# Optimization experiments

Measured on AMD Instinct MI355X. Metric: run time of the kernel, lower is better.

Reference implementation:

```python
import jax, jax.numpy as jnp
import numpy as np

NUM_HEADS = 8
NUM_LANDMARKS = 64
TOPK_LANDMARKS = 4


def setup_inputs() -> dict:
    key = jax.random.key(0)
    k1, k2, k3, k4 = jax.random.split(key, 4)
    B, N, C = 1, 2048, 512
    return {
        "x": jax.random.normal(k1, (B, N, C), jnp.float32),
        "w_qkv": jax.random.normal(k2, (3 * C, C), jnp.float32) * 0.02,
        "w_proj": jax.random.normal(k3, (C, C), jnp.float32) * 0.02,
        "b_proj": jax.random.normal(k4, (C,), jnp.float32) * 0.02,
    }


def reference(x, w_qkv, w_proj, b_proj):
    B, N, C = x.shape
    H = NUM_HEADS
    Dh = C // H
    m = min(NUM_LANDMARKS, N)          # number of segments (torch views (B,H,m,seg,D))
    kl = min(TOPK_LANDMARKS, m)
    scale = Dh ** -0.5

    qkv = (x @ w_qkv.T).reshape(B, N, 3, H, Dh).transpose(2, 0, 3, 1, 4)
    q, k, v = qkv[0], qkv[1], qkv[2]   # each (B,H,N,Dh)

    seg = -(-N // m)                   # segment length = ceil(N/m)
    pad = seg * m - N

    def segmentize(t):
        if pad > 0:
            t = jnp.pad(t, ((0, 0), (0, 0), (0, pad), (0, 0)))
        return t.reshape(B, H, m, seg, Dh)

    k_seg = segmentize(k)              # (B,H,m,seg,Dh)
    v_seg = segmentize(v)

    centroids = k_seg.mean(axis=3)     # (B,H,m,Dh) -- includes pad zeros, as in torch
    route = jnp.einsum('bhnd,bhmd->bhnm', q, centroids) * scale
    _, topk_idx = jax.lax.top_k(route, kl)  # (B,H,N,kl)

    # gather routed segments per query: (B,H,N,kl,seg,Dh)
    gather = jax.vmap(jax.vmap(lambda segs, ix: segs[ix]))
    sel_k = gather(k_seg, topk_idx).reshape(B, H, N, kl * seg, Dh)
    sel_v = gather(v_seg, topk_idx).reshape(B, H, N, kl * seg, Dh)

    attn = jnp.einsum('bhnd,bhnkd->bhnk', q, sel_k) * scale
    attn = jax.nn.softmax(attn, axis=-1)
    out = jnp.einsum('bhnk,bhnkd->bhnd', attn, sel_v)  # (B,H,N,Dh)
    out = out.transpose(0, 2, 1, 3).reshape(B, N, C)
    return out @ w_proj.T + b_proj
```

## Files before the change

kernel.cpp:

```cpp
#include <hip/hip_runtime.h>
#include <hip/hip_bf16.h>
#include <math.h>

#define N_TOK 2048
#define C_DIM 512
#define H_NUM 8
#define DH 64
#define M_LM 64
#define SEG 32
#define KL 4
#define SCALE 0.125f

typedef __attribute__((ext_vector_type(8))) short short8;
typedef __attribute__((ext_vector_type(8))) unsigned short ushort8v;
typedef __attribute__((ext_vector_type(4))) float f32x4;

__device__ inline unsigned short f2bf(float f) {
  unsigned u = __float_as_uint(f);
  u += 0x7FFF + ((u >> 16) & 1);
  return (unsigned short)(u >> 16);
}
__device__ inline float bf2f(unsigned short h) {
  return __uint_as_float(((unsigned)h) << 16);
}

__global__ __launch_bounds__(256) void gemm_qk(
    const float* __restrict__ A, const float* __restrict__ B,
    float* __restrict__ out_q, float* __restrict__ out_k)
{
  __shared__ float As[32][68];
  __shared__ float Bs[32][68];
  int tid = threadIdx.x;
  int tx = tid & 15, ty = tid >> 4;
  int row0 = blockIdx.y << 6;
  int col0 = blockIdx.x << 6;
  float acc[4][4] = {};
  int kk = tid & 31, rr = tid >> 5;

  float pa[8], pb[8];
#pragma unroll
  for (int i = 0; i < 8; i++) {
    pa[i] = A[(size_t)(row0 + rr + i * 8) * 512 + kk];
    pb[i] = B[(size_t)(col0 + rr + i * 8) * 512 + kk];
  }

  for (int k0 = 0; k0 < 512; k0 += 32) {
    __syncthreads();
#pragma unroll
    for (int i = 0; i < 8; i++) {
      As[kk][rr + i * 8] = pa[i];
      Bs[kk][rr + i * 8] = pb[i];
    }
    __syncthreads();
    if (k0 + 32 < 512) {
#pragma unroll
      for (int i = 0; i < 8; i++) {
        pa[i] = A[(size_t)(row0 + rr + i * 8) * 512 + k0 + 32 + kk];
        pb[i] = B[(size_t)(col0 + rr + i * 8) * 512 + k0 + 32 + kk];
      }
    }
#pragma unroll
    for (int kk2 = 0; kk2 < 32; kk2++) {
      float a[4], b[4];
      *(float4*)a = *(const float4*)&As[kk2][ty << 2];
      *(float4*)b = *(const float4*)&Bs[kk2][tx << 2];
#pragma unroll
      for (int i = 0; i < 4; i++)
#pragma unroll
        for (int j = 0; j < 4; j++) acc[i][j] += a[i] * b[j];
    }
  }

  int t = col0 >> 9;
  int h = (col0 >> 6) & 7;
  float* dst = (t == 0) ? out_q : out_k;
#pragma unroll
  for (int i = 0; i < 4; i++) {
    int n = row0 + (ty << 2) + i;
#pragma unroll
    for (int j = 0; j < 4; j++) {
      int d = (tx << 2) + j;
      dst[(size_t)((h << 11) + n) * DH + d] = acc[i][j];
    }
  }
}

__global__ void split3_kernel(const float* __restrict__ x, const float* __restrict__ wv,
                              const float* __restrict__ wp,
                              unsigned short* __restrict__ X2,
                              unsigned short* __restrict__ W2v,
                              unsigned short* __restrict__ WP2)
{
  int idx = blockIdx.x * 256 + threadIdx.x;
  const float* src; unsigned short* dst; int li;
  if (idx < 1048576)      { src = x;  dst = X2;  li = idx; }
  else if (idx < 1310720) { src = wv; dst = W2v; li = idx - 1048576; }
  else                    { src = wp; dst = WP2; li = idx - 1310720; }
  int r = li >> 9, k = li & 511;
  float a = src[li];
  unsigned short h1 = f2bf(a);
  float r1 = a - bf2f(h1);
  dst[(size_t)(r << 10) + k] = h1;
  dst[(size_t)(r << 10) + 512 + k] = f2bf(r1);
}

__global__ __launch_bounds__(256) void gemm_mfma(
    const unsigned short* __restrict__ A2, const unsigned short* __restrict__ B2,
    unsigned short* __restrict__ ov16, float* __restrict__ ofull,
    const float* __restrict__ bias, int ldout, int mode)
{
  __shared__ short Al[4096];
  __shared__ short Bl[4096];
  int tid = threadIdx.x;
  int lane = tid & 63, w = tid >> 6;
  int row0 = blockIdx.y << 6, col0 = blockIdx.x << 6;
  int wr = (w >> 1) * 32, wc = (w & 1) * 32;
  int m_lo = tid & 7, h8 = (tid >> 3) & 7, m_hi = tid >> 6;
  int ms = m_hi * 8 + m_lo;
  int q = lane >> 4, ln = lane & 15;

  f32x4 acc[2][2];
#pragma unroll
  for (int mi = 0; mi < 2; mi++)
#pragma unroll
    for (int ni = 0; ni < 2; ni++)
#pragma unroll
      for (int r = 0; r < 4; r++) acc[mi][ni][r] = 0.0f;

  for (int s = 0; s < 24; s++) {
    int ka = (s < 8) ? s * 64 : (s < 16) ? 512 + (s - 8) * 64 : (s - 16) * 64;
    int kb = (s < 8) ? s * 64 : (s < 16) ? (s - 8) * 64 : 512 + (s - 16) * 64;
    short8 a0 = *(const short8*)(A2 + (size_t)(row0 + ms) * 1024 + ka + h8 * 8);
    short8 a1 = *(const short8*)(A2 + (size_t)(row0 + ms + 32) * 1024 + ka + h8 * 8);
    short8 b0 = *(const short8*)(B2 + (size_t)(col0 + ms) * 1024 + kb + h8 * 8);
    short8 b1 = *(const short8*)(B2 + (size_t)(col0 + ms + 32) * 1024 + kb + h8 * 8);
    __syncthreads();
    *(short8*)&Al[(h8 * 64 + ms) * 8] = a0;
    *(short8*)&Al[(h8 * 64 + ms + 32) * 8] = a1;
    *(short8*)&Bl[(h8 * 64 + ms) * 8] = b0;
    *(short8*)&Bl[(h8 * 64 + ms + 32) * 8] = b1;
    __syncthreads();
    short8 af[2][2], bf[2][2];
#pragma unroll
    for (int sub = 0; sub < 2; sub++)
#pragma unroll
      for (int i = 0; i < 2; i++) {
        af[sub][i] = *(const short8*)&Al[((sub * 4 + q) * 64 + wr + i * 16 + ln) * 8];
        bf[sub][i] = *(const short8*)&Bl[((sub * 4 + q) * 64 + wc + i * 16 + ln) * 8];
      }
#pragma unroll
    for (int sub = 0; sub < 2; sub++)
#pragma unroll
      for (int mi = 0; mi < 2; mi++)
#pragma unroll
        for (int ni = 0; ni < 2; ni++)
          acc[mi][ni] = __builtin_amdgcn_mfma_f32_16x16x32_bf16(
              af[sub][mi], bf[sub][ni], acc[mi][ni], 0, 0, 0);
  }

  if (mode == 0) {
    int hh = (col0 >> 6) & 7;
#pragma unroll
    for (int mi = 0; mi < 2; mi++)
#pragma unroll
      for (int ni = 0; ni < 2; ni++)
#pragma unroll
        for (int r = 0; r < 4; r++) {
          int row = row0 + wr + mi * 16 + q * 4 + r;
          int d = wc + ni * 16 + ln;
          ov16[(size_t)((hh << 11) + row) * DH + d] = f2bf(acc[mi][ni][r]);
        }
  } else {
#pragma unroll
    for (int mi = 0; mi < 2; mi++)
#pragma unroll
      for (int ni = 0; ni < 2; ni++)
#pragma unroll
        for (int r = 0; r < 4; r++) {
          int row = row0 + wr + mi * 16 + q * 4 + r;
          int col = col0 + wc + ni * 16 + ln;
          ofull[(size_t)row * ldout + col] = acc[mi][ni][r] + bias[col];
        }
  }
}

__global__ void centroid_kernel(const float* __restrict__ kb, float* __restrict__ cent)
{
  int idx = blockIdx.x * blockDim.x + threadIdx.x;
  int m = (idx >> 6) & 63;
  int h = idx >> 12;
  int d = idx & 63;
  const float* base = kb + ((size_t)(h << 11) + m * SEG) * DH + d;
  float s = 0.f;
#pragma unroll
  for (int ss = 0; ss < SEG; ss++) s += base[(size_t)ss * DH];
  cent[idx] = s * (1.0f / SEG);
}

__global__ void kbf_kernel(const float* __restrict__ kb, unsigned short* __restrict__ kbf)
{
  int idx = blockIdx.x * 256 + threadIdx.x;
  float4 v = ((const float4*)kb)[idx];
  ushort4 o;
  o.x = f2bf(v.x); o.y = f2bf(v.y); o.z = f2bf(v.z); o.w = f2bf(v.w);
  ((ushort4*)kbf)[idx] = o;
}

__global__ __launch_bounds__(256) void route_topk_kernel(
    const float* __restrict__ qb, const float* __restrict__ cent, int* __restrict__ topk)
{
  __shared__ float centT[64][65];
  __shared__ float qs[4][64];
  int tid = threadIdx.x;
  int wave = tid >> 6, lane = tid & 63;
  int qi = (blockIdx.x << 2) + wave;
  int h = qi >> 11;
  qs[wave][lane] = qb[(size_t)qi * DH + lane];
  const float4* c4 = (const float4*)(cent + ((size_t)h << 12));
#pragma unroll
  for (int i = 0; i < 4; i++) {
    int f4 = tid + 256 * i;
    int m = f4 >> 4;
    int d0 = (f4 & 15) * 4;
    float4 v = c4[f4];
    centT[d0][m] = v.x; centT[d0 + 1][m] = v.y;
    centT[d0 + 2][m] = v.z; centT[d0 + 3][m] = v.w;
  }
  __syncthreads();
  float dot = 0.f;
#pragma unroll
  for (int d = 0; d < 64; d++) dot += qs[wave][d] * centT[d][lane];
  float val = dot * SCALE;
  for (int r = 0; r < KL; r++) {
    float v = val;
    int id = lane;
#pragma unroll
    for (int off = 32; off; off >>= 1) {
      float ov = __shfl_xor(v, off, 64);
      int oi = __shfl_xor(id, off, 64);
      if (ov > v || (ov == v && oi < id)) { v = ov; id = oi; }
    }
    if (lane == 0) topk[qi * KL + r] = id;
    if (lane == id) val = -INFINITY;
  }
}

__global__ __launch_bounds__(256) void attn_kernel(
    const float* __restrict__ qb, const unsigned short* __restrict__ kbf,
    const unsigned short* __restrict__ vbf, const int* __restrict__ topk,
    unsigned short* __restrict__ ao2)
{
  __shared__ float probs[4][132];
  int tid = threadIdx.x;
  int wave = tid >> 6, lane = tid & 63;
  int qi = (blockIdx.x << 2) + wave;
  int h = qi >> 11, n = qi & 2047;
  int4 tk = *(const int4*)(topk + qi * KL);
  int segArr[4] = {tk.x, tk.y, tk.z, tk.w};
  const float* qrow = qb + (size_t)qi * DH;
  float4 qreg[4];
#pragma unroll
  for (int j = 0; j < 2; j++) {
    qreg[j * 2]     = *(const float4*)(qrow + ((lane & 3) + 4 * j) * 8);
    qreg[j * 2 + 1] = *(const float4*)(qrow + ((lane & 3) + 4 * j) * 8 + 4);
  }

  float e[8];
  float score[8];
#pragma unroll
  for (int g = 0; g < 8; g++) {
    int seg = segArr[g >> 1];
    int key_n = seg * SEG + (lane >> 2) + 16 * (g & 1);
    const unsigned short* krow = kbf + ((size_t)(h << 11) + key_n) * DH;
    float a0 = 0.f, a1 = 0.f, a2 = 0.f, a3 = 0.f;
#pragma unroll
    for (int j = 0; j < 2; j++) {
      ushort8v kv = *(const ushort8v*)(krow + ((lane & 3) + 4 * j) * 8);
      float4 q0 = qreg[j * 2], q1 = qreg[j * 2 + 1];
      a0 += q0.x * bf2f(kv[0]); a1 += q0.y * bf2f(kv[1]);
      a2 += q0.z * bf2f(kv[2]); a3 += q0.w * bf2f(kv[3]);
      a0 += q1.x * bf2f(kv[4]); a1 += q1.y * bf2f(kv[5]);
      a2 += q1.z * bf2f(kv[6]); a3 += q1.w * bf2f(kv[7]);
    }
    float acc = (a0 + a1) + (a2 + a3);
    acc += __shfl_xor(acc, 1, 64);
    acc += __shfl_xor(acc, 2, 64);
    score[g] = acc * SCALE;
  }
  float mx = score[0];
#pragma unroll
  for (int g = 1; g < 8; g++) mx = fmaxf(mx, score[g]);
#pragma unroll
  for (int off = 4; off < 64; off <<= 1) mx = fmaxf(mx, __shfl_xor(mx, off, 64));
  float ls = 0.f;
#pragma unroll
  for (int g = 0; g < 8; g++) { e[g] = expf(score[g] - mx); ls += e[g]; }
#pragma unroll
  for (int off = 4; off < 64; off <<= 1) ls += __shfl_xor(ls, off, 64);
  float inv = 1.0f / ls;
  if ((lane & 3) == 0) {
#pragma unroll
    for (int g = 0; g < 8; g++)
      probs[wave][(g >> 1) * 33 + (lane >> 2) + 16 * (g & 1)] = e[g] * inv;
  }
  __syncthreads();

  int gi = lane >> 4, lx = lane & 15;
  int rh = lx >> 3, dl = lx & 7;
  int seg = segArr[gi];
  const unsigned short* vbase = vbf + ((size_t)(h << 11) + seg * SEG) * DH + dl * 8;
  float o[8] = {};
#pragma unroll
  for (int ss = 0; ss < 16; ss++) {
    int row = rh * 16 + ss;
    float p = probs[wave][gi * 33 + row];
    ushort8v vv = *(const ushort8v*)(vbase + (size_t)row * DH);
#pragma unroll
    for (int j = 0; j < 8; j++) o[j] += p * bf2f(vv[j]);
  }
#pragma unroll
  for (int off = 8; off < 64; off <<= 1) {
#pragma unroll
    for (int j = 0; j < 8; j++) o[j] += __shfl_xor(o[j], off, 64);
  }
  if (lane < 8) {
    ushort8v hi8, lo8;
#pragma unroll
    for (int j = 0; j < 8; j++) {
      unsigned short hb = f2bf(o[j]);
      hi8[j] = (short)hb;
      lo8[j] = (short)f2bf(o[j] - bf2f(hb));
    }
    *(ushort8v*)(ao2 + (size_t)n * 1024 + (h << 6) + (lane << 3)) = hi8;
    *(ushort8v*)(ao2 + (size_t)n * 1024 + 512 + (h << 6) + (lane << 3)) = lo8;
  }
}

extern "C" void kernel_launch(void* const* d_in, const int* in_sizes, int n_in,
                              void* d_out, int out_size, void* d_ws, size_t ws_size,
                              hipStream_t stream)
{
  const float* x      = (const float*)d_in[0];
  const float* w_qkv  = (const float*)d_in[1];
  const float* w_proj = (const float*)d_in[2];
  const float* b_proj = (const float*)d_in[3];
  float* out = (float*)d_out;

  float* base = (float*)d_ws;
  float* qbuf = base;
  float* kbuf = base + 1048576;
  unsigned short* vbf = (unsigned short*)(base + 2097152);
  unsigned short* kbf = (unsigned short*)(base + 2097152 + 524288);
  float* cent = base + 3145728;
  int*   topk = (int*)(base + 3178496);
  unsigned short* X2  = (unsigned short*)(base + 3244032);
  unsigned short* W2v = (unsigned short*)(base + 4292608);
  unsigned short* WP2 = (unsigned short*)(base + 4554752);
  unsigned short* AO2 = X2;

  split3_kernel<<<6144, 256, 0, stream>>>(x, w_qkv + 1024 * 512, w_proj,
                                          X2, W2v, WP2);
  {
    dim3 grid(1024 / 64, N_TOK / 64);
    gemm_qk<<<grid, 256, 0, stream>>>(x, w_qkv, qbuf, kbuf);
  }
  {
    dim3 grid(512 / 64, N_TOK / 64);
    gemm_mfma<<<grid, 256, 0, stream>>>(X2, W2v, vbf, nullptr, nullptr, 0, 0);
  }
  centroid_kernel<<<(H_NUM * M_LM * DH) / 256, 256, 0, stream>>>(kbuf, cent);
  kbf_kernel<<<1024, 256, 0, stream>>>(kbuf, kbf);
  route_topk_kernel<<<(H_NUM * N_TOK) / 4, 256, 0, stream>>>(qbuf, cent, topk);
  attn_kernel<<<(H_NUM * N_TOK) / 4, 256, 0, stream>>>(qbuf, kbf, vbf, topk, AO2);
  {
    dim3 grid(C_DIM / 64, N_TOK / 64);
    gemm_mfma<<<grid, 256, 0, stream>>>(AO2, WP2, nullptr, out, b_proj, C_DIM, 1);
  }
}
```

Baseline: 195.8 us.

## Fuse Q/K fp32 GEMM and V MFMA GEMM into one launch, emit bf16 K inline

```diff
diff --git a/kernel.cpp b/kernel.cpp
--- a/kernel.cpp
+++ b/kernel.cpp
@@ -24,64 +24,134 @@
   return __uint_as_float(((unsigned)h) << 16);
 }
 
-__global__ __launch_bounds__(256) void gemm_qk(
+__global__ __launch_bounds__(256) void fused_qkv(
     const float* __restrict__ A, const float* __restrict__ B,
-    float* __restrict__ out_q, float* __restrict__ out_k)
-{
-  __shared__ float As[32][68];
-  __shared__ float Bs[32][68];
+    float* __restrict__ out_q, float* __restrict__ out_k,
+    unsigned short* __restrict__ kbf,
+    const unsigned short* __restrict__ A2, const unsigned short* __restrict__ B2,
+    unsigned short* __restrict__ ov16)
+{
+  __shared__ union {
+    struct { float As[32][68]; float Bs[32][68]; } qk;
+    struct { short Al[4096]; short Bl[4096]; } mf;
+  } lds;
   int tid = threadIdx.x;
-  int tx = tid & 15, ty = tid >> 4;
-  int row0 = blockIdx.y << 6;
-  int col0 = blockIdx.x << 6;
-  float acc[4][4] = {};
-  int kk = tid & 31, rr = tid >> 5;
-
-  float pa[8], pb[8];
-#pragma unroll
-  for (int i = 0; i < 8; i++) {
-    pa[i] = A[(size_t)(row0 + rr + i * 8) * 512 + kk];
-    pb[i] = B[(size_t)(col0 + rr + i * 8) * 512 + kk];
-  }
-
-  for (int k0 = 0; k0 < 512; k0 += 32) {
-    __syncthreads();
+  int bid = blockIdx.x;
+
+  if (bid < 512) {
+    int tx = tid & 15, ty = tid >> 4;
+    int row0 = (bid >> 4) << 6;
+    int col0 = (bid & 15) << 6;
+    float acc[4][4] = {};
+    int kk = tid & 31, rr = tid >> 5;
+
+    float pa[8], pb[8];
 #pragma unroll
     for (int i = 0; i < 8; i++) {
-      As[kk][rr + i * 8] = pa[i];
-      Bs[kk][rr + i * 8] = pb[i];
-    }
-    __syncthreads();
-    if (k0 + 32 < 512) {
+      pa[i] = A[(size_t)(row0 + rr + i * 8) * 512 + kk];
+      pb[i] = B[(size_t)(col0 + rr + i * 8) * 512 + kk];
+    }
+
+    for (int k0 = 0; k0 < 512; k0 += 32) {
+      __syncthreads();
 #pragma unroll
       for (int i = 0; i < 8; i++) {
-        pa[i] = A[(size_t)(row0 + rr + i * 8) * 512 + k0 + 32 + kk];
-        pb[i] = B[(size_t)(col0 + rr + i * 8) * 512 + k0 + 32 + kk];
-      }
-    }
-#pragma unroll
-    for (int kk2 = 0; kk2 < 32; kk2++) {
-      float a[4], b[4];
-      *(float4*)a = *(const float4*)&As[kk2][ty << 2];
-      *(float4*)b = *(const float4*)&Bs[kk2][tx << 2];
-#pragma unroll
-      for (int i = 0; i < 4; i++)
-#pragma unroll
-        for (int j = 0; j < 4; j++) acc[i][j] += a[i] * b[j];
-    }
-  }
-
-  int t = col0 >> 9;
-  int h = (col0 >> 6) & 7;
-  float* dst = (t == 0) ? out_q : out_k;
-#pragma unroll
-  for (int i = 0; i < 4; i++) {
-    int n = row0 + (ty << 2) + i;
-#pragma unroll
-    for (int j = 0; j < 4; j++) {
-      int d = (tx << 2) + j;
-      dst[(size_t)((h << 11) + n) * DH + d] = acc[i][j];
-    }
+        lds.qk.As[kk][rr + i * 8] = pa[i];
+        lds.qk.Bs[kk][rr + i * 8] = pb[i];
+      }
+      __syncthreads();
+      if (k0 + 32 < 512) {
+#pragma unroll
+        for (int i = 0; i < 8; i++) {
+          pa[i] = A[(size_t)(row0 + rr + i * 8) * 512 + k0 + 32 + kk];
+          pb[i] = B[(size_t)(col0 + rr + i * 8) * 512 + k0 + 32 + kk];
+        }
+      }
+#pragma unroll
+      for (int kk2 = 0; kk2 < 32; kk2++) {
+        float a[4], b[4];
+        *(float4*)a = *(const float4*)&lds.qk.As[kk2][ty << 2];
+        *(float4*)b = *(const float4*)&lds.qk.Bs[kk2][tx << 2];
+#pragma unroll
+        for (int i = 0; i < 4; i++)
+#pragma unroll
+          for (int j = 0; j < 4; j++) acc[i][j] += a[i] * b[j];
+      }
+    }
+
+    int t = col0 >> 9;
+    int h = (col0 >> 6) & 7;
+    float* dst = (t == 0) ? out_q : out_k;
+#pragma unroll
+    for (int i = 0; i < 4; i++) {
+      int n = row0 + (ty << 2) + i;
+#pragma unroll
+      for (int j = 0; j < 4; j++) {
+        int d = (tx << 2) + j;
+        float v = acc[i][j];
+        dst[(size_t)((h << 11) + n) * DH + d] = v;
+        if (t == 1) kbf[(size_t)((h << 11) + n) * DH + d] = f2bf(v);
+      }
+    }
+  } else {
+    int idx = bid - 512;
+    int lane = tid & 63, w = tid >> 6;
+    int row0 = (idx >> 3) << 6, col0 = (idx & 7) << 6;
+    int wr = (w >> 1) * 32, wc = (w & 1) * 32;
+    int m_lo = tid & 7, h8 = (tid >> 3) & 7, m_hi = tid >> 6;
+    int ms = m_hi * 8 + m_lo;
+    int q = lane >> 4, ln = lane & 15;
+
+    f32x4 acc[2][2];
+#pragma unroll
+    for (int mi = 0; mi < 2; mi++)
+#pragma unroll
+      for (int ni = 0; ni < 2; ni++)
+#pragma unroll
+        for (int r = 0; r < 4; r++) acc[mi][ni][r] = 0.0f;
+
+    for (int s = 0; s < 24; s++) {
+      int ka = (s < 8) ? s * 64 : (s < 16) ? 512 + (s - 8) * 64 : (s - 16) * 64;
+      int kb = (s < 8) ? s * 64 : (s < 16) ? (s - 8) * 64 : 512 + (s - 16) * 64;
+      short8 a0 = *(const short8*)(A2 + (size_t)(row0 + ms) * 1024 + ka + h8 * 8);
+      short8 a1 = *(const short8*)(A2 + (size_t)(row0 + ms + 32) * 1024 + ka + h8 * 8);
+      short8 b0 = *(const short8*)(B2 + (size_t)(col0 + ms) * 1024 + kb + h8 * 8);
+      short8 b1 = *(const short8*)(B2 + (size_t)(col0 + ms + 32) * 1024 + kb + h8 * 8);
+      __syncthreads();
+      *(short8*)&lds.mf.Al[(h8 * 64 + ms) * 8] = a0;
+      *(short8*)&lds.mf.Al[(h8 * 64 + ms + 32) * 8] = a1;
+      *(short8*)&lds.mf.Bl[(h8 * 64 + ms) * 8] = b0;
+      *(short8*)&lds.mf.Bl[(h8 * 64 + ms + 32) * 8] = b1;
+      __syncthreads();
+      short8 af[2][2], bf[2][2];
+#pragma unroll
+      for (int sub = 0; sub < 2; sub++)
+#pragma unroll
+        for (int i = 0; i < 2; i++) {
+          af[sub][i] = *(const short8*)&lds.mf.Al[((sub * 4 + q) * 64 + wr + i * 16 + ln) * 8];
+          bf[sub][i] = *(const short8*)&lds.mf.Bl[((sub * 4 + q) * 64 + wc + i * 16 + ln) * 8];
+        }
+#pragma unroll
+      for (int sub = 0; sub < 2; sub++)
+#pragma unroll
+        for (int mi = 0; mi < 2; mi++)
+#pragma unroll
+          for (int ni = 0; ni < 2; ni++)
+            acc[mi][ni] = __builtin_amdgcn_mfma_f32_16x16x32_bf16(
+                af[sub][mi], bf[sub][ni], acc[mi][ni], 0, 0, 0);
+    }
+
+    int hh = (col0 >> 6) & 7;
+#pragma unroll
+    for (int mi = 0; mi < 2; mi++)
+#pragma unroll
+      for (int ni = 0; ni < 2; ni++)
+#pragma unroll
+        for (int r = 0; r < 4; r++) {
+          int row = row0 + wr + mi * 16 + q * 4 + r;
+          int d = wc + ni * 16 + ln;
+          ov16[(size_t)((hh << 11) + row) * DH + d] = f2bf(acc[mi][ni][r]);
+        }
   }
 }
 
@@ -106,8 +176,7 @@
 
 __global__ __launch_bounds__(256) void gemm_mfma(
     const unsigned short* __restrict__ A2, const unsigned short* __restrict__ B2,
-    unsigned short* __restrict__ ov16, float* __restrict__ ofull,
-    const float* __restrict__ bias, int ldout, int mode)
+    float* __restrict__ ofull, const float* __restrict__ bias, int ldout)
 {
   __shared__ short Al[4096];
   __shared__ short Bl[4096];
@@ -158,30 +227,16 @@
               af[sub][mi], bf[sub][ni], acc[mi][ni], 0, 0, 0);
   }
 
-  if (mode == 0) {
-    int hh = (col0 >> 6) & 7;
-#pragma unroll
-    for (int mi = 0; mi < 2; mi++)
-#pragma unroll
-      for (int ni = 0; ni < 2; ni++)
-#pragma unroll
-        for (int r = 0; r < 4; r++) {
-          int row = row0 + wr + mi * 16 + q * 4 + r;
-          int d = wc + ni * 16 + ln;
-          ov16[(size_t)((hh << 11) + row) * DH + d] = f2bf(acc[mi][ni][r]);
-        }
-  } else {
-#pragma unroll
-    for (int mi = 0; mi < 2; mi++)
-#pragma unroll
-      for (int ni = 0; ni < 2; ni++)
-#pragma unroll
-        for (int r = 0; r < 4; r++) {
-          int row = row0 + wr + mi * 16 + q * 4 + r;
-          int col = col0 + wc + ni * 16 + ln;
-          ofull[(size_t)row * ldout + col] = acc[mi][ni][r] + bias[col];
-        }
-  }
+#pragma unroll
+  for (int mi = 0; mi < 2; mi++)
+#pragma unroll
+    for (int ni = 0; ni < 2; ni++)
+#pragma unroll
+      for (int r = 0; r < 4; r++) {
+        int row = row0 + wr + mi * 16 + q * 4 + r;
+        int col = col0 + wc + ni * 16 + ln;
+        ofull[(size_t)row * ldout + col] = acc[mi][ni][r] + bias[col];
+      }
 }
 
 __global__ void centroid_kernel(const float* __restrict__ kb, float* __restrict__ cent)
@@ -195,15 +250,6 @@
 #pragma unroll
   for (int ss = 0; ss < SEG; ss++) s += base[(size_t)ss * DH];
   cent[idx] = s * (1.0f / SEG);
-}
-
-__global__ void kbf_kernel(const float* __restrict__ kb, unsigned short* __restrict__ kbf)
-{
-  int idx = blockIdx.x * 256 + threadIdx.x;
-  float4 v = ((const float4*)kb)[idx];
-  ushort4 o;
-  o.x = f2bf(v.x); o.y = f2bf(v.y); o.z = f2bf(v.z); o.w = f2bf(v.w);
-  ((ushort4*)kbf)[idx] = o;
 }
 
 __global__ __launch_bounds__(256) void route_topk_kernel(
@@ -360,20 +406,12 @@
 
   split3_kernel<<<6144, 256, 0, stream>>>(x, w_qkv + 1024 * 512, w_proj,
                                           X2, W2v, WP2);
-  {
-    dim3 grid(1024 / 64, N_TOK / 64);
-    gemm_qk<<<grid, 256, 0, stream>>>(x, w_qkv, qbuf, kbuf);
-  }
-  {
-    dim3 grid(512 / 64, N_TOK / 64);
-    gemm_mfma<<<grid, 256, 0, stream>>>(X2, W2v, vbf, nullptr, nullptr, 0, 0);
-  }
+  fused_qkv<<<768, 256, 0, stream>>>(x, w_qkv, qbuf, kbuf, kbf, X2, W2v, vbf);
   centroid_kernel<<<(H_NUM * M_LM * DH) / 256, 256, 0, stream>>>(kbuf, cent);
-  kbf_kernel<<<1024, 256, 0, stream>>>(kbuf, kbf);
   route_topk_kernel<<<(H_NUM * N_TOK) / 4, 256, 0, stream>>>(qbuf, cent, topk);
   attn_kernel<<<(H_NUM * N_TOK) / 4, 256, 0, stream>>>(qbuf, kbf, vbf, topk, AO2);
   {
     dim3 grid(C_DIM / 64, N_TOK / 64);
-    gemm_mfma<<<grid, 256, 0, stream>>>(AO2, WP2, nullptr, out, b_proj, C_DIM, 1);
-  }
-}
+    gemm_mfma<<<grid, 256, 0, stream>>>(AO2, WP2, out, b_proj, C_DIM);
+  }
+}
```

After: 221.7 us. 1.13x slower.
